# Kernel tuning notes

Hardware: AMD Instinct MI355X
Metric: run time of the kernel (lower is better)

The kernel has to match this reference:

```python
import jax, jax.numpy as jnp
import numpy as np

B, C, H, W = 16, 1, 512, 512
D, F, KH, KW = 4, 24, 5, 5   # numWienerFilters, output_features, reg-filter size
BKH, BKW = 9, 9              # blur kernel size
LB, UB = 1e-4, 1e-2


def psf2otf(psf, shape):
    # zero-pad psf to `shape`, circularly shift its center to (0,0), FFT
    kh, kw = psf.shape[-2], psf.shape[-1]
    pad = [(0, 0)] * (psf.ndim - 2) + [(0, shape[0] - kh), (0, shape[1] - kw)]
    p = jnp.pad(psf, pad)
    p = jnp.roll(p, shift=(-((kh - 1) // 2), -((kw - 1) // 2)), axis=(-2, -1))
    return jnp.fft.fft2(p)


def _taper_profile(proj, n):
    # autocorrelation of the psf projection, periodized to length n (MATLAB edgetaper)
    z = jnp.zeros(n - 1, proj.dtype).at[: proj.shape[0]].set(proj)
    zf = jnp.fft.fft(z)
    acf = jnp.real(jnp.fft.ifft(zf * jnp.conj(zf)))
    acf = jnp.concatenate([acf, acf[:1]])
    return acf / acf.max()


def _normalize_weights(w, scale):
    # WeightNormalization5D: zero-mean + L2-normalize over (C,kh,kw), times scale
    w = w - w.mean(axis=(2, 3, 4), keepdims=True)
    nrm = jnp.sqrt(jnp.sum(w * w, axis=(2, 3, 4), keepdims=True))
    return w * (scale[..., None, None, None] / nrm)


def setup_inputs():
    key = jax.random.key(0)
    ks = jax.random.split(key, 4)
    x = jax.random.uniform(ks[0], (B, C, H, W), jnp.float32)
    bk = jax.random.uniform(ks[1], (BKH, BKW), jnp.float32) + 1e-3
    bk = bk / bk.sum()  # normalized blur PSF
    stdn = jax.random.uniform(ks[2], (B,), jnp.float32) * 0.1 + 0.01
    conv_weights = jax.random.normal(ks[3], (D, F, C, KH, KW), jnp.float32)
    scale = jnp.full((D, F), 0.1, jnp.float32)
    alpha = jnp.log(jnp.logspace(np.log10(LB), np.log10(UB), D))[:, None].astype(jnp.float32)
    return {"x": x, "blur_kernel": bk, "stdn": stdn,
            "conv_weights": conv_weights, "scale": scale, "alpha": alpha}


def reference(x, blur_kernel, stdn, conv_weights, scale, alpha):
    kh, kw = blur_kernel.shape
    # getPad2RetainShape
    pt, pb = (kh + 1) // 2 - 1, kh - (kh + 1) // 2
    pl, pr = (kw + 1) // 2 - 1, kw - (kw + 1) // 2
    xp = jnp.pad(x, ((0, 0), (0, 0), (pt, pb), (pl, pr)), mode="symmetric")
    Hp, Wp = xp.shape[-2], xp.shape[-1]
    otf = psf2otf(blur_kernel, (Hp, Wp))                     # (Hp,Wp) complex
    # EdgeTaper: blend image with its circular blur near borders
    br = _taper_profile(blur_kernel.sum(axis=1), Hp)
    bc = _taper_profile(blur_kernel.sum(axis=0), Wp)
    taper = (1.0 - br)[:, None] * (1.0 - bc)[None, :]
    blurred = jnp.real(jnp.fft.ifft2(jnp.fft.fft2(xp) * otf))
    xp = taper * xp + (1.0 - taper) * blurred
    # regularization-filter OTFs
    w = _normalize_weights(conv_weights, scale)              # (D,F,C,kh,kw)
    G = psf2otf(w, (Hp, Wp))                                 # (D,F,C,Hp,Wp)
    S = jnp.sum(G.real ** 2 + G.imag ** 2, axis=1)           # (D,C,Hp,Wp)
    a = jnp.exp(alpha)[:, :, None, None]                     # (D,1,1,1)
    B2 = otf.real ** 2 + otf.imag ** 2                       # (Hp,Wp)
    denom = B2[None, None] + a * S                           # (D,C,Hp,Wp)
    Y = jnp.conj(otf) * jnp.fft.fft2(xp)                     # (B,C,Hp,Wp)
    Xf = Y[:, None] / denom[None]                            # (B,D,C,Hp,Wp)
    out = jnp.real(jnp.fft.ifft2(Xf))[..., pt:Hp - pb, pl:Wp - pr]
    # colored-noise std factor per (wiener filter, channel)
    cvar = jnp.mean(B2[None, None] / denom ** 2, axis=(-2, -1))   # (D,C)
    cvar = jnp.broadcast_to(cvar[None], (x.shape[0],) + cvar.shape)  # (B,D,C)
    cstdn = jnp.sqrt(stdn[:, None] ** 2 * cvar.mean(axis=2))        # (B,D)
    return out, cstdn
```

## Files before the change

kernel.cpp:

```cpp
#include <hip/hip_runtime.h>
#include <math.h>

#define NP    520
#define NN    (520*520)
#define HH    512
#define NPIX  (512*512)
#define NB    16
#define NPAIR 8
#define ND    4
#define NF    24
#define KS    544
#define RS    576
#define PLANE ((size_t)RS*KS)
#define S8P   (8*PLANE)
#define E9SZ  (NP*9)
#define CSZ   (ND*9*NP)
#define NBORD 18396
#define PADCH 5536
#define NBLK2 1057
#define TWO_PI 6.283185307179586f

typedef unsigned short u16;
typedef __attribute__((ext_vector_type(8))) short bf16x8;
typedef __attribute__((ext_vector_type(4))) float f32x4;

__device__ __forceinline__ int wrap520(int t){ t %= NP; return t < 0 ? t + NP : t; }

__device__ __forceinline__ u16 f2bf(float f){
  unsigned u = __float_as_uint(f);
  u += 0x7FFFu + ((u >> 16) & 1u);
  return (u16)(u >> 16);
}
__device__ __forceinline__ float bf2f(u16 h){
  return __uint_as_float(((unsigned)h) << 16);
}
__device__ __forceinline__ void gll16(const u16* g, u16* l){
  __builtin_amdgcn_global_load_lds(
      (const __attribute__((address_space(1))) void*)g,
      (__attribute__((address_space(3))) void*)l, 16, 0, 0);
}
template<int N> __device__ __forceinline__ void vmwait(){
  if constexpr (N == 0)       asm volatile("s_waitcnt vmcnt(0)" ::: "memory");
  else if constexpr (N == 4)  asm volatile("s_waitcnt vmcnt(4)" ::: "memory");
  else if constexpr (N == 6)  asm volatile("s_waitcnt vmcnt(6)" ::: "memory");
  else if constexpr (N == 8)  asm volatile("s_waitcnt vmcnt(8)" ::: "memory");
  else if constexpr (N == 12) asm volatile("s_waitcnt vmcnt(12)" ::: "memory");
}
#define MF(a,b,c) __builtin_amdgcn_mfma_f32_16x16x32_bf16((a),(b),(c),0,0,0)


__global__ __launch_bounds__(256) void zwb_k(u16* __restrict__ slabs,
                                             u16* __restrict__ wf, u16* __restrict__ wi){
  int idx = blockIdx.x*256 + threadIdx.x;
  const int nA = 16*PADCH;
  if (idx < nA){
    int pl = idx / PADCH, cc = idx % PADCH;
    int row, col;
    if (cc < 1728){ row = cc/3; col = 520 + (cc%3)*8; }
    else { int c2 = cc - 1728; row = 520 + c2/68; col = (c2%68)*8; }
    bf16x8 z = {0,0,0,0,0,0,0,0};
    *(bf16x8*)(slabs + (size_t)pl*PLANE + (size_t)row*KS + col) = z;
    return;
  }
  idx -= nA;
  if (idx >= (int)PLANE) return;
  int r = idx / KS, k = idx % KS;
  float fr=0.f, fi=0.f, ir=0.f, ii=0.f;
  if (r < NP && k < NP){
    int m = (int)(((long long)r * (long long)k) % NP);
    float ang = TWO_PI * (float)m / (float)NP;
    float s, c; sincosf(ang, &s, &c);
    fr = c; fi = -s;
    ir = c * (1.0f/NP); ii = s * (1.0f/NP);
  }
  wf[0*PLANE+idx] = f2bf(fr); wf[1*PLANE+idx] = f2bf(fi);
  wi[0*PLANE+idx] = f2bf(ir); wi[1*PLANE+idx] = f2bf(ii);
}

__global__ __launch_bounds__(256) void setup1_k(const float* __restrict__ bk,
                                                const float* __restrict__ cw,
                                                const float* __restrict__ scale,
                                                float* __restrict__ e9,
                                                float* __restrict__ r_row, float* __restrict__ r_col,
                                                float* __restrict__ wn){
  int idx = blockIdx.x*256 + threadIdx.x;
  if (idx < NP*9){
    int u = idx / 9, t = idx % 9;
    int m = wrap520(u*(t-4));
    float ang = TWO_PI * (float)m / (float)NP;
    float s, c; sincosf(ang, &s, &c);
    e9[idx] = c; e9[E9SZ + idx] = -s;
    return;
  }
  idx -= NP*9;
  if (idx < 18){
    int k = idx % 9;
    bool rowp = (idx < 9);
    float proj[9];
    for (int m = 0; m < 9; ++m){
      float a = 0.f;
      for (int j = 0; j < 9; ++j) a += rowp ? bk[m*9+j] : bk[j*9+m];
      proj[m] = a;
    }
    float acc = 0.f;
    for (int m = 0; m + k < 9; ++m) acc += proj[m] * proj[m+k];
    (rowp ? r_row : r_col)[k] = acc;
    return;
  }
  idx -= 18;
  if (idx >= ND*NF) return;
  const float* wp = cw + idx*25;
  float mean = 0.f;
  for (int k = 0; k < 25; ++k) mean += wp[k];
  mean *= (1.0f/25.0f);
  float ss = 0.f;
  for (int k = 0; k < 25; ++k){ float d = wp[k]-mean; ss += d*d; }
  float sc = scale[idx] / sqrtf(ss);
  for (int k = 0; k < 25; ++k) wn[idx*25+k] = (wp[k]-mean)*sc;
}

__global__ __launch_bounds__(256) void setup2_k(const float* __restrict__ bk,
                                                const float* __restrict__ e9,
                                                const float* __restrict__ wn,
                                                float* __restrict__ T, float* __restrict__ R){
  int idx = blockIdx.x*256 + threadIdx.x;
  if (idx < 9*NP){
    int i = idx / NP, v = idx % NP;
    float tr = 0.f, ti = 0.f;
    #pragma unroll
    for (int j = 0; j < 9; ++j){
      float w = bk[i*9+j];
      tr += w * e9[v*9+j];
      ti += w * e9[E9SZ + v*9+j];
    }
    T[idx] = tr; T[9*NP + idx] = ti;
    return;
  }
  idx -= 9*NP;
  if (idx >= ND*81) return;
  int d = idx / 81, t = idx % 81;
  int di = t/9 - 4, dj = t%9 - 4;
  int i0 = di > 0 ? di : 0, i1 = di < 0 ? 4+di : 4;
  int j0 = dj > 0 ? dj : 0, j1 = dj < 0 ? 4+dj : 4;
  float acc = 0.f;
  for (int f = 0; f < NF; ++f){
    const float* w = wn + (d*NF+f)*25;
    for (int i = i0; i <= i1; ++i)
      for (int j = j0; j <= j1; ++j)
        acc += w[i*5+j] * w[(i-di)*5 + (j-dj)];
  }
  R[idx] = acc;
}

__global__ void C_k(const float* __restrict__ R, const float* __restrict__ e9,
                    float* __restrict__ Ctab){
  int idx = blockIdx.x*blockDim.x + threadIdx.x;
  if (idx >= ND*9*NP) return;
  int v = idx % NP, t9 = idx / NP;
  int d = t9 / 9, t = t9 % 9;
  float cr = 0.f, ci = 0.f;
  #pragma unroll
  for (int s = 0; s < 9; ++s){
    float r = R[d*81 + t*9 + s];
    cr += r * e9[v*9+s];
    ci += r * e9[E9SZ + v*9+s];
  }
  Ctab[idx] = cr; Ctab[CSZ + idx] = ci;
}

__global__ __launch_bounds__(256) void denomMT2_k(
    const float* __restrict__ Tb, const float* __restrict__ e9,
    const float* __restrict__ Ctab, const float* __restrict__ alpha,
    u16* __restrict__ MTre, u16* __restrict__ MTim, float* __restrict__ pcv){
  __shared__ float e9r[2304], e9i[2304];
  __shared__ float tbs[2][2][9];
  __shared__ float cts[2][2][36];
  __shared__ f32x4 red[256];
  const int tid = threadIdx.x;
  const int p0 = blockIdx.x*256;
  const int p = p0 + tid;
  const int v0 = p0 / NP;
  {
    int u0 = p0 % NP;
    for (int i = tid; i < 2304; i += 256){
      int row = i / 9, col = i % 9;
      int uu = u0 + row; if (uu >= NP) uu -= NP;
      e9r[i] = e9[uu*9 + col];
      e9i[i] = e9[E9SZ + uu*9 + col];
    }
    if (tid < 36){
      int s = tid / 18, rem = tid % 18, h = rem / 9, i = rem % 9;
      int vv = v0 + s; if (vv >= NP) vv = NP-1;
      tbs[s][h][i] = Tb[h*(9*NP) + i*NP + vv];
    } else if (tid < 36 + 144){
      int t = tid - 36;
      int s = t / 72, rem = t % 72, h = rem / 36, j = rem % 36;
      int vv = v0 + s; if (vv >= NP) vv = NP-1;
      cts[s][h][j] = Ctab[(size_t)h*CSZ + (size_t)j*NP + vv];
    }
  }
  __syncthreads();
  f32x4 contrib = {0.f, 0.f, 0.f, 0.f};
  if (p < NN){
    int sl = p/NP - v0;
    float er9[9], ei9[9];
    #pragma unroll
    for (int i = 0; i < 9; ++i){ er9[i] = e9r[tid*9+i]; ei9[i] = e9i[tid*9+i]; }
    float ar = 0.f, ai = 0.f;
    #pragma unroll
    for (int i = 0; i < 9; ++i){
      float tr = tbs[sl][0][i], ti = tbs[sl][1][i];
      ar += er9[i]*tr - ei9[i]*ti;
      ai += er9[i]*ti + ei9[i]*tr;
    }
    float B2 = ar*ar + ai*ai;
    #pragma unroll
    for (int d = 0; d < ND; ++d){
      float S = 0.f;
      #pragma unroll
      for (int t = 0; t < 9; ++t)
        S += er9[t]*cts[sl][0][d*9+t] - ei9[t]*cts[sl][1][d*9+t];
      float dv = B2 + expf(alpha[d]) * S;
      MTre[(size_t)d*NN + p] = f2bf(ar / dv);
      MTim[(size_t)d*NN + p] = f2bf(-ai / dv);
      contrib[d] = B2 / (dv*dv);
    }
  }
  red[tid] = contrib; __syncthreads();
  for (int s = 128; s > 0; s >>= 1){
    if (tid < s) red[tid] += red[tid+s];
    __syncthreads();
  }
  if (tid < ND) pcv[(size_t)blockIdx.x*ND + tid] = red[0][tid];
}

__global__ __launch_bounds__(256) void cstdn2_k(const float* __restrict__ stdn,
                                                const float* __restrict__ pcv,
                                                float* __restrict__ out){
  __shared__ float red[256];
  int t = threadIdx.x;
  int d = t & 3, ch = t >> 2;
  float acc = 0.f;
  for (int b = ch; b < NBLK2; b += 64) acc += pcv[(size_t)b*ND + d];
  red[t] = acc; __syncthreads();
  for (int s = 128; s >= 4; s >>= 1){
    if (t < s) red[t] += red[t+s];
    __syncthreads();
  }
  if (t < NB*ND){
    int b = t >> 2, d2 = t & 3;
    float s = stdn[b];
    out[(size_t)NB*ND*NPIX + t] = sqrtf(s*s*red[d2]*(1.0f/(float)NN));
  }
}

__global__ __launch_bounds__(256) void pad_tr_k(const float* __restrict__ x,
                                                u16* __restrict__ MA){
  __shared__ float tile[64][65];
  const int q  = blockIdx.z;
  const int r0 = blockIdx.y * 64;
  const int c0 = blockIdx.x * 64;
  const int t  = threadIdx.x;
  const float* xq = x + (size_t)q*NPIX;
  const int jl = t & 63, ib = t >> 6;
  const bool fast = (c0 >= 64 && c0 <= 448 && r0 >= 64 && r0 <= 448);

  if (fast){
    #pragma unroll 1
    for (int pass = 0; pass < 16; ++pass){
      int il = ib + pass*4;
      tile[il][jl] = xq[(size_t)(c0+il-4)*HH + (r0+jl-4)];
    }
  } else {
    #pragma unroll 1
    for (int pass = 0; pass < 16; ++pass){
      int il = ib + pass*4;
      int I = c0 + il, J = r0 + jl;
      float v = 0.f;
      if (I < NP && J < NP){
        int si = I - 4; si = (si < 0) ? (-si-1) : ((si >= HH) ? (2*HH-1-si) : si);
        int sj = J - 4; sj = (sj < 0) ? (-sj-1) : ((sj >= HH) ? (2*HH-1-sj) : sj);
        v = xq[(size_t)si*HH + sj];
      }
      tile[il][jl] = v;
    }
  }
  __syncthreads();

  const int cchunk = t & 7, rb = t >> 3;
  const int pair = q >> 1, pl = q & 1;
  #pragma unroll
  for (int half = 0; half < 2; ++half){
    int rl = rb + half*32;
    int r = r0 + rl, cg = c0 + cchunk*8;
    if (r >= NP || cg >= NP) continue;
    bf16x8 vh;
    #pragma unroll
    for (int e = 0; e < 8; ++e)
      vh[e] = (short)f2bf(tile[cchunk*8+e][rl]);
    size_t o = (size_t)pair*PLANE + (size_t)r*KS + cg;
    *(bf16x8*)(MA + (size_t)pl*S8P + o) = vh;
  }
}

__global__ __launch_bounds__(256) void border_k(const float* __restrict__ x,
                                                const float* __restrict__ bk,
                                                const float* __restrict__ r_row,
                                                const float* __restrict__ r_col,
                                                u16* __restrict__ MA){
  __shared__ float bks[81], rr_[9], rc_[9];
  if (threadIdx.x < 81) bks[threadIdx.x] = bk[threadIdx.x];
  if (threadIdx.x < 9){ rr_[threadIdx.x] = r_row[threadIdx.x]; rc_[threadIdx.x] = r_col[threadIdx.x]; }
  __syncthreads();
  int idx = blockIdx.x*256 + threadIdx.x;
  if (idx >= NB*NBORD) return;
  int q = idx / NBORD, t = idx % NBORD;
  int I, J;
  if (t < 9360){ int ri = t / 520; I = (ri < 9) ? ri : 502 + ri; J = t % 520; }
  else { int s = t - 9360; I = 9 + s / 18; int ci = s % 18; J = (ci < 9) ? ci : 502 + ci; }
  const float* xq = x + (size_t)q*NPIX;
  auto XP = [&](int ii, int jj)->float{
    int si = ii - 4; si = (si < 0) ? (-si-1) : ((si >= HH) ? (2*HH-1-si) : si);
    int sj = jj - 4; sj = (sj < 0) ? (-sj-1) : ((sj >= HH) ? (2*HH-1-sj) : sj);
    return xq[(size_t)si*HH + sj];
  };
  float v = XP(I, J);
  float brv = (I < 9) ? rr_[I] : ((I >= 511) ? rr_[519-I] : 0.f);
  float bcv = (J < 9) ? rc_[J] : ((J >= 511) ? rc_[519-J] : 0.f);
  brv /= rr_[0]; bcv /= rc_[0];
  float tp = (1.f - brv) * (1.f - bcv);
  float blur = 0.f;
  for (int a = 0; a < 9; ++a){
    int ii = wrap520(I - a + 4);
    for (int b2 = 0; b2 < 9; ++b2){
      int jj = wrap520(J - b2 + 4);
      blur += bks[a*9+b2] * XP(ii, jj);
    }
  }
  v = tp*v + (1.f - tp)*blur;
  int pair = q >> 1, pl = q & 1;
  MA[(size_t)pl*S8P + (size_t)pair*PLANE + (size_t)J*KS + I] = f2bf(v);
}

__global__ __launch_bounds__(256) void maskF_k(const u16* __restrict__ IN, u16* __restrict__ OUT,
                                               const u16* __restrict__ Mre, const u16* __restrict__ Mim){
  int idx = blockIdx.x*256 + threadIdx.x;
  if (idx >= NPAIR*NP*65) return;
  int pr = idx / (NP*65), rem = idx % (NP*65);
  int r = rem / 65, c0 = (rem % 65)*8;
  size_t o = (size_t)pr*PLANE + (size_t)r*KS + c0;
  bf16x8 qr = *(const bf16x8*)(IN + 0*S8P + o);
  bf16x8 qi = *(const bf16x8*)(IN + 1*S8P + o);
  const u16* mrp = Mre + (size_t)r*NP + c0;
  const u16* mip = Mim + (size_t)r*NP + c0;
  bf16x8 o0, o1;
  #pragma unroll
  for (int e = 0; e < 8; ++e){
    float vr = bf2f((u16)qr[e]), vi = bf2f((u16)qi[e]);
    float mr = bf2f(mrp[e]), mi = bf2f(mip[e]);
    o0[e] = (short)f2bf(vr*mr - vi*mi);
    o1[e] = (short)f2bf(vr*mi + vi*mr);
  }
  *(bf16x8*)(OUT + 0*S8P + o) = o0;
  *(bf16x8*)(OUT + 1*S8P + o) = o1;
}

template<int BM, int CROP, int MASKOUT>
__global__ __launch_bounds__(256) void gemm_k(
    const u16* __restrict__ P, size_t pPl, size_t pZp, size_t pZd,
    const u16* __restrict__ Q, size_t qPl, size_t qZp, size_t qZd,
    u16* __restrict__ O, size_t oPl, size_t oZp, size_t oZd,
    float* __restrict__ cropOut, int dBase,
    const u16* __restrict__ Mre, const u16* __restrict__ Mim)
{
  constexpr int NW = 4;
  constexpr int FR = BM/32;
  constexpr int TR = BM/16;
  constexpr int LPW = 4*TR/NW;
  constexpr int PLSTR = BM*32;
  constexpr int BUF = 4*PLSTR;
  constexpr int NK = KS/32;
  __shared__ u16 lds[3*BUF];
  const int tid = threadIdx.x;
  const int l = tid & 63, w = tid >> 6;

  const int gx = gridDim.x, gy = gridDim.y;
  int lin = blockIdx.x + gx*(blockIdx.y + gy*blockIdx.z);
  int ntot = gx*gy*gridDim.z;
  int q8 = ntot >> 3, r8 = ntot & 7;
  int xcd = lin & 7, id8 = lin >> 3;
  int nl = (xcd < r8 ? xcd*(q8+1) : r8*(q8+1) + (xcd-r8)*q8) + id8;
  int BX = nl % gx; int t2 = nl / gx;
  int BY = t2 % gy; int BZ = t2 / gy;

  const int pair = BZ & 7;
  const int dd = dBase + (BZ >> 3);
  const int R0 = BY * BM, C0 = BX * BM;

  const u16* Pb = P + (size_t)pair*pZp + (size_t)dd*pZd;
  const u16* Qb = Q + (size_t)pair*qZp + (size_t)dd*qZd;

  const int s = l >> 2;
  const int cs8 = ((l & 3) ^ ((s >> 1) & 3)) * 8;
  const size_t pOff0 = (size_t)(R0 + s)*KS + cs8;
  const size_t qOff0 = (size_t)(C0 + s)*KS + cs8;

  const int lm = l & 15, lc = l >> 4;
  const int wm = w >> 1, wn = w & 1;

  f32x4 zero4 = {0.f, 0.f, 0.f, 0.f};
  f32x4 aRe[FR][FR], aIm[FR][FR];
  #pragma unroll
  for (int i = 0; i < FR; ++i)
    #pragma unroll
    for (int j = 0; j < FR; ++j){ aRe[i][j] = zero4; aIm[i][j] = zero4; }

  auto STAGE = [&](int bi, int k0){
    u16* dst = lds + bi*BUF;
    #pragma unroll
    for (int i = 0; i < LPW; ++i){
      int t = w + i*NW;
      int q2 = t / TR, r2 = t % TR;
      const u16* src = (q2 < 2) ? (Pb + (size_t)q2*pPl + pOff0)
                                : (Qb + (size_t)(q2-2)*qPl + qOff0);
      gll16(src + (size_t)(r2*16)*KS + k0, dst + q2*PLSTR + r2*512);
    }
  };

  STAGE(0, 0);
  STAGE(1, 32);

  #pragma unroll 1
  for (int kt = 0; kt < NK; ++kt){
    if (kt + 1 < NK) vmwait<LPW>(); else vmwait<0>();
    __builtin_amdgcn_sched_barrier(0);
    __builtin_amdgcn_s_barrier();
    __builtin_amdgcn_sched_barrier(0);

    const u16* buf = lds + (kt%3)*BUF;
    bf16x8 pf[FR][2];
    #pragma unroll
    for (int mi = 0; mi < FR; ++mi){
      int r = wm*(FR*16) + mi*16 + lm;
      int co = ((lc ^ ((r >> 1) & 3)) << 3);
      pf[mi][0] = *(const bf16x8*)(buf + 0*PLSTR + r*32 + co);
      pf[mi][1] = *(const bf16x8*)(buf + 1*PLSTR + r*32 + co);
    }
    #pragma unroll
    for (int ni = 0; ni < FR; ++ni){
      int rq = wn*(FR*16) + ni*16 + lm;
      int cq = ((lc ^ ((rq >> 1) & 3)) << 3);
      bf16x8 q0 = *(const bf16x8*)(buf + 2*PLSTR + rq*32 + cq);
      bf16x8 q1 = *(const bf16x8*)(buf + 3*PLSTR + rq*32 + cq);
      if (ni == 0){
        if (kt + 2 < NK) STAGE((kt+2)%3, (kt+2)*32);
      } else {
        __builtin_amdgcn_sched_barrier(0);
        __builtin_amdgcn_s_barrier();
      }
      asm volatile("s_waitcnt lgkmcnt(0)" ::: "memory");
      __builtin_amdgcn_sched_barrier(0);
      __builtin_amdgcn_s_setprio(1);
      #pragma unroll
      for (int mi = 0; mi < FR; ++mi){
        bf16x8 nw = pf[mi][1] ^ (short)0x8000;
        f32x4 re = aRe[mi][ni], im = aIm[mi][ni];
        re = MF(pf[mi][0], q0, re);
        re = MF(nw,        q1, re);
        im = MF(pf[mi][0], q1, im);
        im = MF(pf[mi][1], q0, im);
        aRe[mi][ni] = re; aIm[mi][ni] = im;
      }
      __builtin_amdgcn_s_setprio(0);
    }
  }

  u16* Ob = O ? (O + (size_t)pair*oZp + (size_t)dd*oZd) : nullptr;
  #pragma unroll
  for (int mi = 0; mi < FR; ++mi)
    #pragma unroll
    for (int ni = 0; ni < FR; ++ni){
      int cb = C0 + wn*(FR*16) + ni*16 + lm;
      int rb = R0 + wm*(FR*16) + mi*16 + lc*4;
      #pragma unroll
      for (int e = 0; e < 4; ++e){
        int rr = rb + e;
        float vr = aRe[mi][ni][e], vi = aIm[mi][ni][e];
        if (CROP){
          if (rr >= 4 && rr < 516 && cb >= 4 && cb < 516){
            size_t px = (size_t)(rr-4)*HH + (cb-4);
            cropOut[((size_t)(2*pair  )*ND + dd)*NPIX + px] = vr;
            cropOut[((size_t)(2*pair+1)*ND + dd)*NPIX + px] = vi;
          }
        } else if (MASKOUT){
          if (cb < KS){
            size_t o = (size_t)rr*KS + cb;
            size_t mo = (size_t)(rr < NP ? rr : 0)*NP + (cb < NP ? cb : 0);
            #pragma unroll
            for (int d2 = 0; d2 < ND; ++d2){
              float mr = bf2f(Mre[(size_t)d2*NN + mo]);
              float mi2 = bf2f(Mim[(size_t)d2*NN + mo]);
              u16* Od = O + (size_t)d2*oZd + (size_t)pair*oZp;
              Od[0*oPl+o] = f2bf(vr*mr - vi*mi2);
              Od[1*oPl+o] = f2bf(vr*mi2 + vi*mr);
            }
          }
        } else {
          if (cb < KS){
            size_t o = (size_t)rr*KS + cb;
            Ob[0*oPl+o] = f2bf(vr);
            Ob[1*oPl+o] = f2bf(vi);
          }
        }
      }
    }
}


extern "C" void kernel_launch(void* const* d_in, const int* in_sizes, int n_in,
                              void* d_out, int out_size, void* d_ws, size_t ws_size,
                              hipStream_t stream){
  const float* x     = (const float*)d_in[0];
  const float* bk    = (const float*)d_in[1];
  const float* stdn  = (const float*)d_in[2];
  const float* cw    = (const float*)d_in[3];
  const float* scale = (const float*)d_in[4];
  const float* alpha = (const float*)d_in[5];
  float* out = (float*)d_out;

  char* base = (char*)d_ws;
  const size_t UNIT = 16*PLANE*sizeof(u16);
  size_t off;
  auto alloc = [&](size_t bytes)->void*{
    void* p = base + off;
    off += (bytes + 255) & ~(size_t)255;
    return p;
  };

  u16 *MA, *MB, *MC, *Dm, *Do, *WF, *WI, *MTre, *MTim;
  float *e9, *Tb, *Rarr, *Ctab, *r_row, *r_col, *wn, *pcv;
  auto layout = [&](bool bigL){
    off = 0;
    MA = (u16*)alloc(UNIT);
    MB = (u16*)alloc(UNIT);
    if (bigL){ Dm = (u16*)alloc(4*UNIT); Do = (u16*)alloc(4*UNIT); MC = nullptr; }
    else     { MC = (u16*)alloc(UNIT);   Dm = nullptr; Do = nullptr; }
    WF = (u16*)alloc(2*PLANE*sizeof(u16));
    WI = (u16*)alloc(2*PLANE*sizeof(u16));
    MTre = (u16*)alloc((size_t)ND*NN*2);
    MTim = (u16*)alloc((size_t)ND*NN*2);
    e9   = (float*)alloc(2*E9SZ*4);
    Tb   = (float*)alloc(2*9*NP*4);
    Rarr = (float*)alloc(ND*81*4);
    Ctab = (float*)alloc(2*CSZ*4);
    r_row = (float*)alloc(64);
    r_col = (float*)alloc(64);
    wn   = (float*)alloc(ND*NF*25*4);
    pcv  = (float*)alloc((size_t)NBLK2*ND*4);
    return off;
  };
  bool big = (layout(true) <= ws_size);
  if (!big){
    if (layout(false) > ws_size) return;
  }

  {
    int ztot = 16*PADCH + (int)PLANE;
    zwb_k<<<(ztot+255)/256, 256, 0, stream>>>(MA, WF, WI);
  }
  setup1_k<<<(NP*9+18+ND*NF+255)/256, 256, 0, stream>>>(bk, cw, scale, e9, r_row, r_col, wn);
  setup2_k<<<(9*NP+ND*81+255)/256, 256, 0, stream>>>(bk, e9, wn, Tb, Rarr);
  C_k     <<<(ND*9*NP+255)/256, 256, 0, stream>>>(Rarr, e9, Ctab);
  denomMT2_k<<<NBLK2, 256, 0, stream>>>(Tb, e9, Ctab, alpha, MTre, MTim, pcv);
  cstdn2_k<<<1, 256, 0, stream>>>(stdn, pcv, out);
  pad_tr_k<<<dim3(9, 9, NB), 256, 0, stream>>>(x, MA);
  border_k<<<(NB*NBORD+255)/256, 256, 0, stream>>>(x, bk, r_row, r_col, MA);

  gemm_k<64,0,0><<<dim3(9,9,8),256,0,stream>>>(
      WF, PLANE, 0, 0,   MA, S8P, PLANE, 0,   MB, S8P, PLANE, 0,
      nullptr, 0, nullptr, nullptr);

  if (big){
    gemm_k<64,0,1><<<dim3(9,9,8),256,0,stream>>>(
        WF, PLANE, 0, 0,   MB, S8P, PLANE, 0,   Dm, S8P, PLANE, 16*PLANE,
        nullptr, 0, MTre, MTim);
    gemm_k<96,0,0><<<dim3(6,6,32),256,0,stream>>>(
        WI, PLANE, 0, 0,   Dm, S8P, PLANE, 16*PLANE,   Do, S8P, PLANE, 16*PLANE,
        nullptr, 0, nullptr, nullptr);
    gemm_k<96,1,0><<<dim3(6,6,32),256,0,stream>>>(
        Do, S8P, PLANE, 16*PLANE,   WI, PLANE, 0, 0,   nullptr, 0, 0, 0,
        out, 0, nullptr, nullptr);
  } else {
    gemm_k<64,0,0><<<dim3(9,9,8),256,0,stream>>>(
        WF, PLANE, 0, 0,   MB, S8P, PLANE, 0,   MC, S8P, PLANE, 0,
        nullptr, 0, nullptr, nullptr);
    const int mgrid = (NPAIR*NP*65 + 255)/256;
    for (int d = 0; d < ND; ++d){
      maskF_k<<<mgrid,256,0,stream>>>(MC, MA, MTre + (size_t)d*NN, MTim + (size_t)d*NN);
      gemm_k<96,0,0><<<dim3(6,6,8),256,0,stream>>>(
          WI, PLANE, 0, 0,   MA, S8P, PLANE, 0,   MB, S8P, PLANE, 0,
          nullptr, 0, nullptr, nullptr);
      gemm_k<96,1,0><<<dim3(6,6,8),256,0,stream>>>(
          MB, S8P, PLANE, 0,   WI, PLANE, 0, 0,   nullptr, 0, 0, 0,
          out, d, nullptr, nullptr);
    }
  }
}
```

Before: 269.8 us.

## Merge setup and pad/border kernels, recompute twiddles inline instead of e9 table

Folds the zero/twiddle, setup1 and setup2 kernels into one setup kernel and merges the padding-transpose and border-taper kernels into one launch. The e9 twiddle table and the normalized-weight buffer are dropped, and sincos factors are recomputed inline in setup, C_k and denomMT2_k. The border region is redrawn so the two merged parts write disjoint areas of the padded image. This cuts launch count and inter-kernel dependencies, at the cost of extra sincos work and a redundant per-thread weight normalization in the R computation.

```diff
diff --git a/kernel.cpp b/kernel.cpp
--- a/kernel.cpp
+++ b/kernel.cpp
@@ -13,11 +13,10 @@
 #define RS    576
 #define PLANE ((size_t)RS*KS)
 #define S8P   (8*PLANE)
-#define E9SZ  (NP*9)
-#define CSZ   (ND*9*NP)
-#define NBORD 18396
+#define NBORD2 25424
 #define PADCH 5536
 #define NBLK2 1057
+#define CSZ   (ND*9*NP)
 #define TWO_PI 6.283185307179586f
 
 typedef unsigned short u16;
@@ -48,9 +47,13 @@
 }
 #define MF(a,b,c) __builtin_amdgcn_mfma_f32_16x16x32_bf16((a),(b),(c),0,0,0)
 
-
-__global__ __launch_bounds__(256) void zwb_k(u16* __restrict__ slabs,
-                                             u16* __restrict__ wf, u16* __restrict__ wi){
+__global__ __launch_bounds__(256) void setup_k(const float* __restrict__ bk,
+                                               const float* __restrict__ cw,
+                                               const float* __restrict__ scale,
+                                               u16* __restrict__ slabs,
+                                               u16* __restrict__ wf, u16* __restrict__ wi,
+                                               float* __restrict__ r_row, float* __restrict__ r_col,
+                                               float* __restrict__ T, float* __restrict__ R){
   int idx = blockIdx.x*256 + threadIdx.x;
   const int nA = 16*PADCH;
   if (idx < nA){
@@ -63,36 +66,21 @@
     return;
   }
   idx -= nA;
-  if (idx >= (int)PLANE) return;
-  int r = idx / KS, k = idx % KS;
-  float fr=0.f, fi=0.f, ir=0.f, ii=0.f;
-  if (r < NP && k < NP){
-    int m = (int)(((long long)r * (long long)k) % NP);
-    float ang = TWO_PI * (float)m / (float)NP;
-    float s, c; sincosf(ang, &s, &c);
-    fr = c; fi = -s;
-    ir = c * (1.0f/NP); ii = s * (1.0f/NP);
-  }
-  wf[0*PLANE+idx] = f2bf(fr); wf[1*PLANE+idx] = f2bf(fi);
-  wi[0*PLANE+idx] = f2bf(ir); wi[1*PLANE+idx] = f2bf(ii);
-}
-
-__global__ __launch_bounds__(256) void setup1_k(const float* __restrict__ bk,
-                                                const float* __restrict__ cw,
-                                                const float* __restrict__ scale,
-                                                float* __restrict__ e9,
-                                                float* __restrict__ r_row, float* __restrict__ r_col,
-                                                float* __restrict__ wn){
-  int idx = blockIdx.x*256 + threadIdx.x;
-  if (idx < NP*9){
-    int u = idx / 9, t = idx % 9;
-    int m = wrap520(u*(t-4));
-    float ang = TWO_PI * (float)m / (float)NP;
-    float s, c; sincosf(ang, &s, &c);
-    e9[idx] = c; e9[E9SZ + idx] = -s;
+  if (idx < (int)PLANE){
+    int r = idx / KS, k = idx % KS;
+    float fr=0.f, fi=0.f, ir=0.f, ii=0.f;
+    if (r < NP && k < NP){
+      int m = (int)(((long long)r * (long long)k) % NP);
+      float ang = TWO_PI * (float)m / (float)NP;
+      float s, c; sincosf(ang, &s, &c);
+      fr = c; fi = -s;
+      ir = c * (1.0f/NP); ii = s * (1.0f/NP);
+    }
+    wf[0*PLANE+idx] = f2bf(fr); wf[1*PLANE+idx] = f2bf(fi);
+    wi[0*PLANE+idx] = f2bf(ir); wi[1*PLANE+idx] = f2bf(ii);
     return;
   }
-  idx -= NP*9;
+  idx -= (int)PLANE;
   if (idx < 18){
     int k = idx % 9;
     bool rowp = (idx < 9);
@@ -108,30 +96,16 @@
     return;
   }
   idx -= 18;
-  if (idx >= ND*NF) return;
-  const float* wp = cw + idx*25;
-  float mean = 0.f;
-  for (int k = 0; k < 25; ++k) mean += wp[k];
-  mean *= (1.0f/25.0f);
-  float ss = 0.f;
-  for (int k = 0; k < 25; ++k){ float d = wp[k]-mean; ss += d*d; }
-  float sc = scale[idx] / sqrtf(ss);
-  for (int k = 0; k < 25; ++k) wn[idx*25+k] = (wp[k]-mean)*sc;
-}
-
-__global__ __launch_bounds__(256) void setup2_k(const float* __restrict__ bk,
-                                                const float* __restrict__ e9,
-                                                const float* __restrict__ wn,
-                                                float* __restrict__ T, float* __restrict__ R){
-  int idx = blockIdx.x*256 + threadIdx.x;
   if (idx < 9*NP){
     int i = idx / NP, v = idx % NP;
     float tr = 0.f, ti = 0.f;
     #pragma unroll
     for (int j = 0; j < 9; ++j){
+      int m = wrap520(v*(j-4));
+      float ang = TWO_PI * (float)m / (float)NP;
+      float s, c; sincosf(ang, &s, &c);
       float w = bk[i*9+j];
-      tr += w * e9[v*9+j];
-      ti += w * e9[E9SZ + v*9+j];
+      tr += w * c; ti += w * (-s);
     }
     T[idx] = tr; T[9*NP + idx] = ti;
     return;
@@ -144,16 +118,23 @@
   int j0 = dj > 0 ? dj : 0, j1 = dj < 0 ? 4+dj : 4;
   float acc = 0.f;
   for (int f = 0; f < NF; ++f){
-    const float* w = wn + (d*NF+f)*25;
+    const float* wp = cw + (d*NF+f)*25;
+    float mean = 0.f;
+    for (int k = 0; k < 25; ++k) mean += wp[k];
+    mean *= (1.0f/25.0f);
+    float ss = 0.f;
+    for (int k = 0; k < 25; ++k){ float dv = wp[k]-mean; ss += dv*dv; }
+    float sc = scale[d*NF+f] / sqrtf(ss);
+    float part = 0.f;
     for (int i = i0; i <= i1; ++i)
       for (int j = j0; j <= j1; ++j)
-        acc += w[i*5+j] * w[(i-di)*5 + (j-dj)];
+        part += (wp[i*5+j]-mean) * (wp[(i-di)*5 + (j-dj)]-mean);
+    acc += sc*sc*part;
   }
   R[idx] = acc;
 }
 
-__global__ void C_k(const float* __restrict__ R, const float* __restrict__ e9,
-                    float* __restrict__ Ctab){
+__global__ void C_k(const float* __restrict__ R, float* __restrict__ Ctab){
   int idx = blockIdx.x*blockDim.x + threadIdx.x;
   if (idx >= ND*9*NP) return;
   int v = idx % NP, t9 = idx / NP;
@@ -161,18 +142,20 @@
   float cr = 0.f, ci = 0.f;
   #pragma unroll
   for (int s = 0; s < 9; ++s){
+    int m = wrap520(v*(s-4));
+    float ang = TWO_PI * (float)m / (float)NP;
+    float sn, cs; sincosf(ang, &sn, &cs);
     float r = R[d*81 + t*9 + s];
-    cr += r * e9[v*9+s];
-    ci += r * e9[E9SZ + v*9+s];
+    cr += r * cs;
+    ci += r * (-sn);
   }
   Ctab[idx] = cr; Ctab[CSZ + idx] = ci;
 }
 
 __global__ __launch_bounds__(256) void denomMT2_k(
-    const float* __restrict__ Tb, const float* __restrict__ e9,
-    const float* __restrict__ Ctab, const float* __restrict__ alpha,
+    const float* __restrict__ Tb, const float* __restrict__ Ctab,
+    const float* __restrict__ alpha,
     u16* __restrict__ MTre, u16* __restrict__ MTim, float* __restrict__ pcv){
-  __shared__ float e9r[2304], e9i[2304];
   __shared__ float tbs[2][2][9];
   __shared__ float cts[2][2][36];
   __shared__ f32x4 red[256];
@@ -181,13 +164,6 @@
   const int p = p0 + tid;
   const int v0 = p0 / NP;
   {
-    int u0 = p0 % NP;
-    for (int i = tid; i < 2304; i += 256){
-      int row = i / 9, col = i % 9;
-      int uu = u0 + row; if (uu >= NP) uu -= NP;
-      e9r[i] = e9[uu*9 + col];
-      e9i[i] = e9[E9SZ + uu*9 + col];
-    }
     if (tid < 36){
       int s = tid / 18, rem = tid % 18, h = rem / 9, i = rem % 9;
       int vv = v0 + s; if (vv >= NP) vv = NP-1;
@@ -202,10 +178,16 @@
   __syncthreads();
   f32x4 contrib = {0.f, 0.f, 0.f, 0.f};
   if (p < NN){
+    int u = p % NP;
     int sl = p/NP - v0;
     float er9[9], ei9[9];
     #pragma unroll
-    for (int i = 0; i < 9; ++i){ er9[i] = e9r[tid*9+i]; ei9[i] = e9i[tid*9+i]; }
+    for (int i = 0; i < 9; ++i){
+      int m = wrap520(u*(i-4));
+      float ang = TWO_PI * (float)m / (float)NP;
+      float sn, cs; sincosf(ang, &sn, &cs);
+      er9[i] = cs; ei9[i] = -sn;
+    }
     float ar = 0.f, ai = 0.f;
     #pragma unroll
     for (int i = 0; i < 9; ++i){
@@ -254,70 +236,82 @@
   }
 }
 
-__global__ __launch_bounds__(256) void pad_tr_k(const float* __restrict__ x,
-                                                u16* __restrict__ MA){
-  __shared__ float tile[64][65];
-  const int q  = blockIdx.z;
-  const int r0 = blockIdx.y * 64;
-  const int c0 = blockIdx.x * 64;
-  const int t  = threadIdx.x;
-  const float* xq = x + (size_t)q*NPIX;
-  const int jl = t & 63, ib = t >> 6;
-  const bool fast = (c0 >= 64 && c0 <= 448 && r0 >= 64 && r0 <= 448);
-
-  if (fast){
-    #pragma unroll 1
-    for (int pass = 0; pass < 16; ++pass){
-      int il = ib + pass*4;
-      tile[il][jl] = xq[(size_t)(c0+il-4)*HH + (r0+jl-4)];
-    }
-  } else {
-    #pragma unroll 1
-    for (int pass = 0; pass < 16; ++pass){
-      int il = ib + pass*4;
-      int I = c0 + il, J = r0 + jl;
-      float v = 0.f;
-      if (I < NP && J < NP){
-        int si = I - 4; si = (si < 0) ? (-si-1) : ((si >= HH) ? (2*HH-1-si) : si);
-        int sj = J - 4; sj = (sj < 0) ? (-sj-1) : ((sj >= HH) ? (2*HH-1-sj) : sj);
-        v = xq[(size_t)si*HH + sj];
+__global__ __launch_bounds__(256) void pb_k(const float* __restrict__ x,
+                                            const float* __restrict__ bk,
+                                            const float* __restrict__ r_row,
+                                            const float* __restrict__ r_col,
+                                            u16* __restrict__ MA){
+  const int PBLK = 9*9*NB;
+  if ((int)blockIdx.x < PBLK){
+    __shared__ float tile[64][65];
+    const int b  = blockIdx.x;
+    const int q  = b / 81;
+    const int by = (b / 9) % 9;
+    const int bx = b % 9;
+    const int r0 = by * 64;
+    const int c0 = bx * 64;
+    const int t  = threadIdx.x;
+    const float* xq = x + (size_t)q*NPIX;
+    const int jl = t & 63, ib = t >> 6;
+    const bool fast = (c0 >= 64 && c0 <= 448 && r0 >= 64 && r0 <= 448);
+
+    if (fast){
+      #pragma unroll 1
+      for (int pass = 0; pass < 16; ++pass){
+        int il = ib + pass*4;
+        tile[il][jl] = xq[(size_t)(c0+il-4)*HH + (r0+jl-4)];
       }
-      tile[il][jl] = v;
-    }
-  }
-  __syncthreads();
-
-  const int cchunk = t & 7, rb = t >> 3;
-  const int pair = q >> 1, pl = q & 1;
-  #pragma unroll
-  for (int half = 0; half < 2; ++half){
-    int rl = rb + half*32;
-    int r = r0 + rl, cg = c0 + cchunk*8;
-    if (r >= NP || cg >= NP) continue;
-    bf16x8 vh;
-    #pragma unroll
-    for (int e = 0; e < 8; ++e)
-      vh[e] = (short)f2bf(tile[cchunk*8+e][rl]);
-    size_t o = (size_t)pair*PLANE + (size_t)r*KS + cg;
-    *(bf16x8*)(MA + (size_t)pl*S8P + o) = vh;
-  }
-}
-
-__global__ __launch_bounds__(256) void border_k(const float* __restrict__ x,
-                                                const float* __restrict__ bk,
-                                                const float* __restrict__ r_row,
-                                                const float* __restrict__ r_col,
-                                                u16* __restrict__ MA){
+    } else {
+      #pragma unroll 1
+      for (int pass = 0; pass < 16; ++pass){
+        int il = ib + pass*4;
+        int I = c0 + il, J = r0 + jl;
+        float v = 0.f;
+        if (I < NP && J < NP){
+          int si = I - 4; si = (si < 0) ? (-si-1) : ((si >= HH) ? (2*HH-1-si) : si);
+          int sj = J - 4; sj = (sj < 0) ? (-sj-1) : ((sj >= HH) ? (2*HH-1-sj) : sj);
+          v = xq[(size_t)si*HH + sj];
+        }
+        tile[il][jl] = v;
+      }
+    }
+    __syncthreads();
+
+    const int cchunk = t & 7, rb = t >> 3;
+    const int pair = q >> 1, pl = q & 1;
+    #pragma unroll
+    for (int half = 0; half < 2; ++half){
+      int rl = rb + half*32;
+      int r = r0 + rl, cg = c0 + cchunk*8;
+      if (r < 9 || r >= 511 || cg < 16 || cg >= 504) continue;
+      bf16x8 vh;
+      #pragma unroll
+      for (int e = 0; e < 8; ++e)
+        vh[e] = (short)f2bf(tile[cchunk*8+e][rl]);
+      size_t o = (size_t)pair*PLANE + (size_t)r*KS + cg;
+      *(bf16x8*)(MA + (size_t)pl*S8P + o) = vh;
+    }
+    return;
+  }
+
   __shared__ float bks[81], rr_[9], rc_[9];
   if (threadIdx.x < 81) bks[threadIdx.x] = bk[threadIdx.x];
   if (threadIdx.x < 9){ rr_[threadIdx.x] = r_row[threadIdx.x]; rc_[threadIdx.x] = r_col[threadIdx.x]; }
   __syncthreads();
-  int idx = blockIdx.x*256 + threadIdx.x;
-  if (idx >= NB*NBORD) return;
-  int q = idx / NBORD, t = idx % NBORD;
+  int idx = ((int)blockIdx.x - PBLK)*256 + threadIdx.x;
+  if (idx >= NB*NBORD2) return;
+  int q = idx / NBORD2, t = idx % NBORD2;
   int I, J;
-  if (t < 9360){ int ri = t / 520; I = (ri < 9) ? ri : 502 + ri; J = t % 520; }
-  else { int s = t - 9360; I = 9 + s / 18; int ci = s % 18; J = (ci < 9) ? ci : 502 + ci; }
+  if (t < 9360){
+    int ji = t / 520;
+    J = (ji < 9) ? ji : 502 + ji;
+    I = t % 520;
+  } else {
+    int s = t - 9360;
+    int iI = s / 502;
+    J = 9 + s % 502;
+    I = (iI < 16) ? iI : 488 + iI;
+  }
   const float* xq = x + (size_t)q*NPIX;
   auto XP = [&](int ii, int jj)->float{
     int si = ii - 4; si = (si < 0) ? (-si-1) : ((si >= HH) ? (2*HH-1-si) : si);
@@ -325,19 +319,21 @@
     return xq[(size_t)si*HH + sj];
   };
   float v = XP(I, J);
-  float brv = (I < 9) ? rr_[I] : ((I >= 511) ? rr_[519-I] : 0.f);
-  float bcv = (J < 9) ? rc_[J] : ((J >= 511) ? rc_[519-J] : 0.f);
-  brv /= rr_[0]; bcv /= rc_[0];
-  float tp = (1.f - brv) * (1.f - bcv);
-  float blur = 0.f;
-  for (int a = 0; a < 9; ++a){
-    int ii = wrap520(I - a + 4);
-    for (int b2 = 0; b2 < 9; ++b2){
-      int jj = wrap520(J - b2 + 4);
-      blur += bks[a*9+b2] * XP(ii, jj);
-    }
-  }
-  v = tp*v + (1.f - tp)*blur;
+  if (I < 9 || I >= 511 || J < 9 || J >= 511){
+    float brv = (I < 9) ? rr_[I] : ((I >= 511) ? rr_[519-I] : 0.f);
+    float bcv = (J < 9) ? rc_[J] : ((J >= 511) ? rc_[519-J] : 0.f);
+    brv /= rr_[0]; bcv /= rc_[0];
+    float tp = (1.f - brv) * (1.f - bcv);
+    float blur = 0.f;
+    for (int a = 0; a < 9; ++a){
+      int ii = wrap520(I - a + 4);
+      for (int b2 = 0; b2 < 9; ++b2){
+        int jj = wrap520(J - b2 + 4);
+        blur += bks[a*9+b2] * XP(ii, jj);
+      }
+    }
+    v = tp*v + (1.f - tp)*blur;
+  }
   int pair = q >> 1, pl = q & 1;
   MA[(size_t)pl*S8P + (size_t)pair*PLANE + (size_t)J*KS + I] = f2bf(v);
 }
@@ -538,7 +534,7 @@
   };
 
   u16 *MA, *MB, *MC, *Dm, *Do, *WF, *WI, *MTre, *MTim;
-  float *e9, *Tb, *Rarr, *Ctab, *r_row, *r_col, *wn, *pcv;
+  float *Tb, *Rarr, *Ctab, *r_row, *r_col, *pcv;
   auto layout = [&](bool bigL){
     off = 0;
     MA = (u16*)alloc(UNIT);
@@ -549,13 +545,11 @@
     WI = (u16*)alloc(2*PLANE*sizeof(u16));
     MTre = (u16*)alloc((size_t)ND*NN*2);
     MTim = (u16*)alloc((size_t)ND*NN*2);
-    e9   = (float*)alloc(2*E9SZ*4);
     Tb   = (float*)alloc(2*9*NP*4);
     Rarr = (float*)alloc(ND*81*4);
     Ctab = (float*)alloc(2*CSZ*4);
     r_row = (float*)alloc(64);
     r_col = (float*)alloc(64);
-    wn   = (float*)alloc(ND*NF*25*4);
     pcv  = (float*)alloc((size_t)NBLK2*ND*4);
     return off;
   };
@@ -565,16 +559,17 @@
   }
 
   {
-    int ztot = 16*PADCH + (int)PLANE;
-    zwb_k<<<(ztot+255)/256, 256, 0, stream>>>(MA, WF, WI);
-  }
-  setup1_k<<<(NP*9+18+ND*NF+255)/256, 256, 0, stream>>>(bk, cw, scale, e9, r_row, r_col, wn);
-  setup2_k<<<(9*NP+ND*81+255)/256, 256, 0, stream>>>(bk, e9, wn, Tb, Rarr);
-  C_k     <<<(ND*9*NP+255)/256, 256, 0, stream>>>(Rarr, e9, Ctab);
-  denomMT2_k<<<NBLK2, 256, 0, stream>>>(Tb, e9, Ctab, alpha, MTre, MTim, pcv);
+    int ztot = 16*PADCH + (int)PLANE + 18 + 9*NP + ND*81;
+    setup_k<<<(ztot+255)/256, 256, 0, stream>>>(bk, cw, scale, MA, WF, WI,
+                                                r_row, r_col, Tb, Rarr);
+  }
+  C_k     <<<(ND*9*NP+255)/256, 256, 0, stream>>>(Rarr, Ctab);
+  denomMT2_k<<<NBLK2, 256, 0, stream>>>(Tb, Ctab, alpha, MTre, MTim, pcv);
   cstdn2_k<<<1, 256, 0, stream>>>(stdn, pcv, out);
-  pad_tr_k<<<dim3(9, 9, NB), 256, 0, stream>>>(x, MA);
-  border_k<<<(NB*NBORD+255)/256, 256, 0, stream>>>(x, bk, r_row, r_col, MA);
+  {
+    int pbBlocks = 9*9*NB + (NB*NBORD2 + 255)/256;
+    pb_k<<<pbBlocks, 256, 0, stream>>>(x, bk, r_row, r_col, MA);
+  }
 
   gemm_k<64,0,0><<<dim3(9,9,8),256,0,stream>>>(
       WF, PLANE, 0, 0,   MA, S8P, PLANE, 0,   MB, S8P, PLANE, 0,
```

Result: slower. 301.6 us (+11.8%).
